# Kernel optimization log

Hardware: AMD Instinct MI355X
Metric: run time of the kernel (lower is better)

## Reference

```python
import jax, jax.numpy as jnp
import numpy as np
from jax.scipy.stats import norm

N = 6144
D1, D2 = 3000, 1000
H = 128          # hardcoded hidden in VAEEncoder
LAT = 64
E = 16           # num_experts
K = 2            # top-k
NOISE_EPS = 0.01
BN_EPS = 1e-5


def setup_inputs() -> dict:
    key = jax.random.key(0)
    ks = jax.random.split(key, 24)
    xav = lambda k, i, o: jax.random.uniform(k, (i, o), jnp.float32,
                                             -np.sqrt(6.0 / (i + o)), np.sqrt(6.0 / (i + o)))
    u = jax.random.uniform(ks[0], (N, N), jnp.float32)
    adj = u / u.sum(axis=1, keepdims=True)  # row-normalized dense graph
    inp = {
        'x1': jax.random.normal(ks[1], (N, D1), jnp.float32),
        'x2': jax.random.normal(ks[2], (N, D2), jnp.float32),
        'adj': adj,
        # modality-1 VAE encoder
        'W1': xav(ks[3], D1, H), 'gamma1': jnp.ones((H,)), 'beta1': jnp.zeros((H,)),
        'Wmu1': xav(ks[4], H, LAT), 'bmu1': jnp.zeros((LAT,)),
        'Wlv1': xav(ks[5], H, LAT), 'blv1': jnp.zeros((LAT,)),
        # modality-2 VAE encoder
        'W2': xav(ks[6], D2, H), 'gamma2': jnp.ones((H,)), 'beta2': jnp.zeros((H,)),
        'Wmu2': xav(ks[7], H, LAT), 'bmu2': jnp.zeros((LAT,)),
        'Wlv2': xav(ks[8], H, LAT), 'blv2': jnp.zeros((LAT,)),
        # MoE gating (torch inits these to zero; small randn gives a non-degenerate baseline)
        'w_gate': 0.02 * jax.random.normal(ks[9], (LAT, E), jnp.float32),
        'w_noise': 0.02 * jax.random.normal(ks[10], (LAT, E), jnp.float32),
        # modality decoders
        'Wd1': xav(ks[11], LAT, LAT), 'Wfc1': xav(ks[12], LAT, D1), 'bfc1': jnp.zeros((D1,)),
        'Wd2': xav(ks[13], LAT, LAT), 'Wfc2': xav(ks[14], LAT, D2), 'bfc2': jnp.zeros((D2,)),
    }
    return inp


def _encode(x, adj, W, gamma, beta, Wmu, bmu, Wlv, blv):
    h = adj @ (x @ W)                                   # [N,H] GNN embed
    mu_b = h.mean(0)
    var_b = h.var(0)
    h = (h - mu_b) / jnp.sqrt(var_b + BN_EPS) * gamma + beta  # BatchNorm1d (train mode)
    return h @ Wmu + bmu, h @ Wlv + blv                 # mu, logvar [N,LAT]


def _cv_squared(v):
    return v.var(ddof=1) / (v.mean() ** 2 + 1e-10)


def _moe_gating(z, w_gate, w_noise, key):
    clean = z @ w_gate                                  # [N,E]
    std = jax.nn.softplus(z @ w_noise) + NOISE_EPS
    noisy = clean + jax.random.normal(key, clean.shape, clean.dtype) * std
    top_vals, top_idx = jax.lax.top_k(noisy, K + 1)     # [N,K+1]
    topk_gates = jax.nn.softmax(top_vals[:, :K], axis=1)
    rows = jnp.arange(z.shape[0])[:, None]
    gates = jnp.zeros_like(clean).at[rows, top_idx[:, :K]].set(topk_gates)
    # differentiable load estimate (prob each expert is in top-k)
    thr_in = top_vals[:, K][:, None]
    thr_out = top_vals[:, K - 1][:, None]
    is_in = noisy > thr_in
    prob = jnp.where(is_in, norm.cdf((clean - thr_in) / std), norm.cdf((clean - thr_out) / std))
    load = prob.sum(0)
    importance = gates.sum(0)
    loss = _cv_squared(importance) + _cv_squared(load)
    return gates, loss


def _decode(z, adj, Wd, Wfc, bfc):
    return (adj @ (z @ Wd)) @ Wfc + bfc                 # Decoder: mm, mm, Linear


def reference(x1, x2, adj,
              W1, gamma1, beta1, Wmu1, bmu1, Wlv1, blv1,
              W2, gamma2, beta2, Wmu2, bmu2, Wlv2, blv2,
              w_gate, w_noise,
              Wd1, Wfc1, bfc1, Wd2, Wfc2, bfc2):
    mu1, lv1 = _encode(x1, adj, W1, gamma1, beta1, Wmu1, bmu1, Wlv1, blv1)
    mu2, lv2 = _encode(x2, adj, W2, gamma2, beta2, Wmu2, bmu2, Wlv2, blv2)
    # Product of Experts over the 2 modalities
    mus = jnp.stack([mu1, mu2], 0)
    lvs = jnp.stack([lv1, lv2], 0)
    var = jnp.exp(lvs) + 1e-8
    T = 1.0 / (var + 1e-8)
    pd_mu = (mus * T).sum(0) / T.sum(0)
    pd_logvar = jnp.log(1.0 / T.sum(0) + 1e-8)
    z = pd_mu
    gates, moe_loss = _moe_gating(z, w_gate, w_noise, jax.random.key(42))
    recon1 = _decode(z, adj, Wd1, Wfc1, bfc1)
    recon2 = _decode(z, adj, Wd2, Wfc2, bfc2)
    return recon1, recon2, pd_mu, pd_logvar, gates, moe_loss
```

## Files before the change

### kernel.cpp

```cpp
#include <hip/hip_runtime.h>
#include <math.h>

#define NR    6144
#define DIM1  3000
#define DIM2  1000
#define HID   128
#define LATD  64
#define NEXP  16

typedef __bf16 bf16x8 __attribute__((ext_vector_type(8)));
typedef float  f32x4  __attribute__((ext_vector_type(4)));

__device__ __forceinline__ unsigned short f2bf_rne(float x) {
  unsigned u = __float_as_uint(x);
  u += 0x7FFFu + ((u >> 16) & 1u);
  return (unsigned short)(u >> 16);
}
__device__ __forceinline__ void split2(float v, unsigned short& h, unsigned short& l) {
  h = f2bf_rne(v);
  float hf = __uint_as_float((unsigned)h << 16);
  l = f2bf_rne(v - hf);
}

template<bool SPLIT3, bool ATOMIC>
__global__ __launch_bounds__(256, 2) void gemm_mfma(
    const float* __restrict__ A,
    const unsigned short* __restrict__ BTh,
    const unsigned short* __restrict__ BTl,
    const float* __restrict__ bias,
    float* __restrict__ C,
    int M, int N, int K, int lda, int Kpad, int ldc, int kchunk)
{
  constexpr int LSZ = 128 * 32;
  __shared__ alignas(16) unsigned short Ah[LSZ];
  __shared__ alignas(16) unsigned short Bh[LSZ];
  __shared__ alignas(16) unsigned short Al[SPLIT3 ? LSZ : 8];
  __shared__ alignas(16) unsigned short Bl[SPLIT3 ? LSZ : 8];

  const int tid  = threadIdx.x;
  const int lane = tid & 63;
  const int wave = tid >> 6;
  const int wm = wave >> 1, wn = wave & 1;
  const int lrow = lane & 15, kg = lane >> 4;

  const int bm = blockIdx.x * 128;
  const int bn = blockIdx.y * 128;
  const int k0 = blockIdx.z * kchunk;
  const int kend = min(k0 + kchunk, K);
  const int nsteps = (kend - k0 + 31) >> 5;

  f32x4 acc[4][4];
  #pragma unroll
  for (int f = 0; f < 4; ++f)
    #pragma unroll
    for (int g = 0; g < 4; ++g)
      #pragma unroll
      for (int j = 0; j < 4; ++j) acc[f][g][j] = 0.f;

  const int srow  = tid >> 1;
  const int ks    = (tid & 1) * 16;
  const int slot0 = (tid & 1) * 2;
  const float* aRow = A + (size_t)(bm + srow) * lda;
  const int gn = bn + srow;
  const bool bvalid = gn < N;
  const unsigned short* bRowH = BTh + (size_t)(bvalid ? gn : 0) * Kpad;
  const unsigned short* bRowL = SPLIT3 ? (BTl + (size_t)(bvalid ? gn : 0) * Kpad) : BTh;

  const int aw0 = srow * 32 + (((slot0    ) ^ (srow & 3)) * 8);
  const int aw1 = srow * 32 + (((slot0 + 1) ^ (srow & 3)) * 8);

  for (int s = 0; s < nsteps; ++s) {
    const int gk = k0 + s * 32;
    const int kb = gk + ks;

    float v[16];
    if (kb + 16 <= kend) {
      const float4* ap = (const float4*)(aRow + kb);
      #pragma unroll
      for (int q = 0; q < 4; ++q) {
        float4 f4 = ap[q];
        v[4*q+0] = f4.x; v[4*q+1] = f4.y; v[4*q+2] = f4.z; v[4*q+3] = f4.w;
      }
    } else {
      #pragma unroll
      for (int i = 0; i < 16; ++i) v[i] = (kb + i < kend) ? aRow[kb + i] : 0.f;
    }
    unsigned hw[8], lw[8];
    #pragma unroll
    for (int i = 0; i < 8; ++i) {
      unsigned short h0, l0, h1, l1;
      split2(v[2*i], h0, l0);
      split2(v[2*i+1], h1, l1);
      hw[i] = (unsigned)h0 | ((unsigned)h1 << 16);
      lw[i] = (unsigned)l0 | ((unsigned)l1 << 16);
    }

    uint4 bh0 = make_uint4(0,0,0,0), bh1 = bh0, bl0 = bh0, bl1 = bh0;
    if (bvalid) {
      const uint4* bp = (const uint4*)(bRowH + gk + ks);
      bh0 = bp[0]; bh1 = bp[1];
      if (SPLIT3) {
        const uint4* bq = (const uint4*)(bRowL + gk + ks);
        bl0 = bq[0]; bl1 = bq[1];
      }
    }

    __syncthreads();
    *(uint4*)&Ah[aw0] = make_uint4(hw[0], hw[1], hw[2], hw[3]);
    *(uint4*)&Ah[aw1] = make_uint4(hw[4], hw[5], hw[6], hw[7]);
    *(uint4*)&Bh[aw0] = bh0;
    *(uint4*)&Bh[aw1] = bh1;
    if (SPLIT3) {
      *(uint4*)&Al[aw0] = make_uint4(lw[0], lw[1], lw[2], lw[3]);
      *(uint4*)&Al[aw1] = make_uint4(lw[4], lw[5], lw[6], lw[7]);
      *(uint4*)&Bl[aw0] = bl0;
      *(uint4*)&Bl[aw1] = bl1;
    }
    __syncthreads();

    bf16x8 afh[4], bfh[4], afl[4], bfl[4];
    #pragma unroll
    for (int f = 0; f < 4; ++f) {
      const int r   = wm * 64 + f * 16 + lrow;
      const int off = r * 32 + ((kg ^ (r & 3)) * 8);
      afh[f] = *(const bf16x8*)&Ah[off];
      const int n    = wn * 64 + f * 16 + lrow;
      const int offb = n * 32 + ((kg ^ (n & 3)) * 8);
      bfh[f] = *(const bf16x8*)&Bh[offb];
      if (SPLIT3) {
        afl[f] = *(const bf16x8*)&Al[off];
        bfl[f] = *(const bf16x8*)&Bl[offb];
      }
    }
    #pragma unroll
    for (int f = 0; f < 4; ++f)
      #pragma unroll
      for (int g = 0; g < 4; ++g) {
        acc[f][g] = __builtin_amdgcn_mfma_f32_16x16x32_bf16(afh[f], bfh[g], acc[f][g], 0, 0, 0);
        if constexpr (SPLIT3) {
          acc[f][g] = __builtin_amdgcn_mfma_f32_16x16x32_bf16(afl[f], bfh[g], acc[f][g], 0, 0, 0);
          acc[f][g] = __builtin_amdgcn_mfma_f32_16x16x32_bf16(afh[f], bfl[g], acc[f][g], 0, 0, 0);
        }
      }
  }

  #pragma unroll
  for (int f = 0; f < 4; ++f) {
    #pragma unroll
    for (int g = 0; g < 4; ++g) {
      const int row0 = bm + wm * 64 + f * 16 + (lane >> 4) * 4;
      const int col  = bn + wn * 64 + g * 16 + (lane & 15);
      if (col < N) {
        #pragma unroll
        for (int j = 0; j < 4; ++j) {
          const size_t idx = (size_t)(row0 + j) * ldc + col;
          if (ATOMIC) atomicAdd(&C[idx], acc[f][g][j]);
          else        C[idx] = acc[f][g][j] + (bias ? bias[col] : 0.f);
        }
      }
    }
  }
}

__global__ __launch_bounds__(256) void transpose_split(
    const float* __restrict__ in, unsigned short* __restrict__ out_hi,
    unsigned short* __restrict__ out_lo, int K, int N, int Kpad)
{
  __shared__ float tile[32][33];
  const int k0 = blockIdx.x * 32, n0 = blockIdx.y * 32;
  const int tx = threadIdx.x & 31, ty = threadIdx.x >> 5;
  #pragma unroll
  for (int r = 0; r < 4; ++r) {
    const int k = k0 + ty + r * 8;
    tile[ty + r * 8][tx] = (k < K && n0 + tx < N) ? in[(size_t)k * N + n0 + tx] : 0.f;
  }
  __syncthreads();
  #pragma unroll
  for (int r = 0; r < 4; ++r) {
    const int nn = ty + r * 8;
    const int n = n0 + nn, k = k0 + tx;
    if (n < N && k < Kpad) {
      unsigned short h, l;
      split2(tile[tx][nn], h, l);
      out_hi[(size_t)n * Kpad + k] = h;
      if (out_lo) out_lo[(size_t)n * Kpad + k] = l;
    }
  }
}

#define BM 64
#define BN 64
#define BK 16

__global__ __launch_bounds__(256) void gemm_f32(
    const float* __restrict__ A, const float* __restrict__ B,
    const float* __restrict__ bias, float* __restrict__ C,
    int M, int N, int K, int lda, int ldb, int ldc)
{
  __shared__ float At[BK][BM + 4];
  __shared__ float Bt[BK][BN + 4];
  const int tid = threadIdx.x;
  const int tx = tid & 15;
  const int ty = tid >> 4;
  const int bm = blockIdx.x * BM;
  const int bn = blockIdx.y * BN;

  float acc[4][4] = {};

  const int ar = tid >> 2;
  const int ak = (tid & 3) * 4;
  const int bk = tid >> 4;
  const int bc = (tid & 15) * 4;

  for (int k0 = 0; k0 < K; k0 += BK) {
    {
      float4 v = make_float4(0.f, 0.f, 0.f, 0.f);
      const int gr = bm + ar;
      const int gk = k0 + ak;
      if (gr < M && gk < K) {
        const float* p = &A[(size_t)gr * lda];
        if (gk + 3 < K) v = *reinterpret_cast<const float4*>(&p[gk]);
        else {
          v.x = p[gk];
          if (gk + 1 < K) v.y = p[gk + 1];
          if (gk + 2 < K) v.z = p[gk + 2];
        }
      }
      At[ak + 0][ar] = v.x; At[ak + 1][ar] = v.y;
      At[ak + 2][ar] = v.z; At[ak + 3][ar] = v.w;
    }
    {
      float4 v = make_float4(0.f, 0.f, 0.f, 0.f);
      const int gk = k0 + bk;
      const int gc = bn + bc;
      if (gk < K) {
        const float* p = &B[(size_t)gk * ldb];
        if (gc + 3 < N) v = *reinterpret_cast<const float4*>(&p[gc]);
        else {
          if (gc     < N) v.x = p[gc];
          if (gc + 1 < N) v.y = p[gc + 1];
          if (gc + 2 < N) v.z = p[gc + 2];
        }
      }
      *reinterpret_cast<float4*>(&Bt[bk][bc]) = v;
    }
    __syncthreads();
    #pragma unroll
    for (int kk = 0; kk < BK; ++kk) {
      float4 a4 = *reinterpret_cast<const float4*>(&At[kk][ty * 4]);
      float4 b4 = *reinterpret_cast<const float4*>(&Bt[kk][tx * 4]);
      float av[4] = {a4.x, a4.y, a4.z, a4.w};
      float bv[4] = {b4.x, b4.y, b4.z, b4.w};
      #pragma unroll
      for (int i = 0; i < 4; ++i)
        #pragma unroll
        for (int j = 0; j < 4; ++j)
          acc[i][j] = fmaf(av[i], bv[j], acc[i][j]);
    }
    __syncthreads();
  }

  #pragma unroll
  for (int i = 0; i < 4; ++i) {
    const int row = bm + ty * 4 + i;
    if (row >= M) continue;
    #pragma unroll
    for (int j = 0; j < 4; ++j) {
      const int col = bn + tx * 4 + j;
      if (col < N) {
        float v = acc[i][j];
        if (bias) v += bias[col];
        C[(size_t)row * ldc + col] = v;
      }
    }
  }
}

__global__ __launch_bounds__(256) void bnstats_kernel(
    const float* __restrict__ H2, float* __restrict__ ssum, float* __restrict__ ssq)
{
  const int c = threadIdx.x;
  const int r0 = blockIdx.x * 12;
  float s = 0.f, q = 0.f;
  #pragma unroll
  for (int i = 0; i < 12; ++i) {
    float v = H2[(size_t)(r0 + i) * 256 + c];
    s += v;
    q = fmaf(v, v, q);
  }
  atomicAdd(&ssum[c], s);
  atomicAdd(&ssq[c], q);
}

__global__ __launch_bounds__(256) void mulv_kernel(
    const float* __restrict__ H2, const float* __restrict__ ssum, const float* __restrict__ ssq,
    const float* __restrict__ g1, const float* __restrict__ b1,
    const float* __restrict__ Wmu1, const float* __restrict__ bmu1,
    const float* __restrict__ Wlv1, const float* __restrict__ blv1,
    const float* __restrict__ g2, const float* __restrict__ b2,
    const float* __restrict__ Wmu2, const float* __restrict__ bmu2,
    const float* __restrict__ Wlv2, const float* __restrict__ blv2,
    float* __restrict__ pd_mu_out, float* __restrict__ pd_lv_out, float* __restrict__ z_out)
{
  __shared__ float hn[4][256];
  const int tid = threadIdx.x;
  const int r0 = blockIdx.x * 4;

  for (int idx = tid; idx < 1024; idx += 256) {
    const int rr = idx >> 8;
    const int c  = idx & 255;
    const float mean = ssum[c] * (1.0f / 6144.0f);
    const float var  = ssq[c] * (1.0f / 6144.0f) - mean * mean;
    const float rstd = 1.0f / sqrtf(var + 1e-5f);
    const float gamma = (c < HID) ? g1[c] : g2[c - HID];
    const float beta  = (c < HID) ? b1[c] : b2[c - HID];
    const float v = H2[(size_t)(r0 + rr) * 256 + c];
    hn[rr][c] = (v - mean) * rstd * gamma + beta;
  }
  __syncthreads();

  const int rr = tid >> 6;
  const int j  = tid & 63;
  float mu1 = bmu1[j], lv1 = blv1[j], mu2 = bmu2[j], lv2 = blv2[j];
  #pragma unroll 4
  for (int k = 0; k < HID; ++k) {
    const float h1 = hn[rr][k];
    const float h2 = hn[rr][HID + k];
    mu1 = fmaf(h1, Wmu1[k * LATD + j], mu1);
    lv1 = fmaf(h1, Wlv1[k * LATD + j], lv1);
    mu2 = fmaf(h2, Wmu2[k * LATD + j], mu2);
    lv2 = fmaf(h2, Wlv2[k * LATD + j], lv2);
  }
  const float var1 = expf(lv1) + 1e-8f;
  const float var2 = expf(lv2) + 1e-8f;
  const float T1 = 1.0f / (var1 + 1e-8f);
  const float T2 = 1.0f / (var2 + 1e-8f);
  const float denom = T1 + T2;
  const float pmu = (mu1 * T1 + mu2 * T2) / denom;
  const float plv = logf(1.0f / denom + 1e-8f);
  const size_t o = (size_t)(r0 + rr) * LATD + j;
  pd_mu_out[o] = pmu;
  pd_lv_out[o] = plv;
  z_out[o]     = pmu;
}

__device__ __forceinline__ unsigned rotl32(unsigned x, int r) {
  return (x << r) | (x >> (32 - r));
}

__device__ float threefry_normal(unsigned i) {
  const unsigned ks0 = 0u;
  const unsigned ks1 = 42u;
  const unsigned ks2 = 0x1BD11BDAu ^ 0u ^ 42u;
  unsigned x0 = 0u + ks0;
  unsigned x1 = i + ks1;

  #define TF_ROUND(r) { x0 += x1; x1 = rotl32(x1, r); x1 ^= x0; }
  TF_ROUND(13) TF_ROUND(15) TF_ROUND(26) TF_ROUND(6)
  x0 += ks1; x1 += ks2 + 1u;
  TF_ROUND(17) TF_ROUND(29) TF_ROUND(16) TF_ROUND(24)
  x0 += ks2; x1 += ks0 + 2u;
  TF_ROUND(13) TF_ROUND(15) TF_ROUND(26) TF_ROUND(6)
  x0 += ks0; x1 += ks1 + 3u;
  TF_ROUND(17) TF_ROUND(29) TF_ROUND(16) TF_ROUND(24)
  x0 += ks1; x1 += ks2 + 4u;
  TF_ROUND(13) TF_ROUND(15) TF_ROUND(26) TF_ROUND(6)
  x0 += ks2; x1 += ks0 + 5u;
  #undef TF_ROUND

  const unsigned bits = x0 ^ x1;

  const unsigned fb = (bits >> 9) | 0x3F800000u;
  const float u01 = __uint_as_float(fb) - 1.0f;
  const float minval = -0.99999994f;
  float u = fmaf(u01, 2.0f, minval);
  u = fmaxf(minval, u);

  float w = -log1pf(-u * u);
  float p;
  if (w < 5.0f) {
    w = w - 2.5f;
    p = 2.81022636e-08f;
    p = fmaf(p, w, 3.43273939e-07f);
    p = fmaf(p, w, -3.5233877e-06f);
    p = fmaf(p, w, -4.39150654e-06f);
    p = fmaf(p, w, 0.00021858087f);
    p = fmaf(p, w, -0.00125372503f);
    p = fmaf(p, w, -0.00417768164f);
    p = fmaf(p, w, 0.246640727f);
    p = fmaf(p, w, 1.50140941f);
  } else {
    w = sqrtf(w) - 3.0f;
    p = -0.000200214257f;
    p = fmaf(p, w, 0.000100950558f);
    p = fmaf(p, w, 0.00134934322f);
    p = fmaf(p, w, -0.00367342844f);
    p = fmaf(p, w, 0.00573950773f);
    p = fmaf(p, w, -0.0076224613f);
    p = fmaf(p, w, 0.00943887047f);
    p = fmaf(p, w, 1.00167406f);
    p = fmaf(p, w, 2.83297682f);
  }
  return 1.4142135f * (p * u);
}

__global__ __launch_bounds__(64) void gating_kernel(
    const float* __restrict__ z, const float* __restrict__ w_gate,
    const float* __restrict__ w_noise, float* __restrict__ gates_out,
    float* __restrict__ importance, float* __restrict__ loadv)
{
  __shared__ float zt[64][65];
  __shared__ float wg[64][16];
  __shared__ float wn[64][16];
  __shared__ float imp_s[16];
  __shared__ float load_s[16];

  const int tid = threadIdx.x;
  const int r0 = blockIdx.x * 64;

  for (int idx = tid; idx < 1024; idx += 64) {
    wg[idx >> 4][idx & 15] = w_gate[idx];
    wn[idx >> 4][idx & 15] = w_noise[idx];
  }
  for (int idx = tid; idx < 4096; idx += 64) {
    const int rr = idx >> 6, c = idx & 63;
    zt[rr][c] = z[(size_t)(r0 + rr) * 64 + c];
  }
  if (tid < 16) { imp_s[tid] = 0.f; load_s[tid] = 0.f; }
  __syncthreads();

  const int r = r0 + tid;
  float clean[16], noisy[16], stdv[16];
  #pragma unroll
  for (int e = 0; e < NEXP; ++e) {
    float c = 0.f, n = 0.f;
    #pragma unroll 8
    for (int k = 0; k < 64; ++k) {
      const float zv = zt[tid][k];
      c = fmaf(zv, wg[k][e], c);
      n = fmaf(zv, wn[k][e], n);
    }
    clean[e] = c;
    const float sp = fmaxf(n, 0.f) + log1pf(expf(-fabsf(n)));
    stdv[e] = sp + 0.01f;
    const float eps = threefry_normal((unsigned)r * 16u + (unsigned)e);
    noisy[e] = fmaf(eps, stdv[e], c);
  }

  float v0 = -1e30f, v1 = -1e30f, v2 = -1e30f;
  int i0 = 0, i1 = 0;
  #pragma unroll
  for (int e = 0; e < NEXP; ++e) {
    const float v = noisy[e];
    if (v > v0)      { v2 = v1; v1 = v0; i1 = i0; v0 = v; i0 = e; }
    else if (v > v1) { v2 = v1; v1 = v; i1 = e; }
    else if (v > v2) { v2 = v; }
  }

  const float e1 = expf(v1 - v0);
  const float inv = 1.0f / (1.0f + e1);
  const float g0 = inv;
  const float g1v = e1 * inv;

  float lacc[16];
  #pragma unroll
  for (int e = 0; e < NEXP; ++e) {
    const float gv = (e == i0) ? g0 : ((e == i1) ? g1v : 0.f);
    gates_out[(size_t)r * NEXP + e] = gv;
    const float thr = (noisy[e] > v2) ? v2 : v1;
    const float x = (clean[e] - thr) / stdv[e];
    lacc[e] = 0.5f * erfcf(-0.70710678f * x);
  }
  atomicAdd(&imp_s[i0], g0);
  atomicAdd(&imp_s[i1], g1v);
  #pragma unroll
  for (int e = 0; e < NEXP; ++e) atomicAdd(&load_s[e], lacc[e]);
  __syncthreads();
  if (tid < 16) {
    atomicAdd(&importance[tid], imp_s[tid]);
    atomicAdd(&loadv[tid], load_s[tid]);
  }
}

__global__ void loss_kernel(const float* __restrict__ imp, const float* __restrict__ ld,
                            float* __restrict__ out)
{
  if (threadIdx.x == 0 && blockIdx.x == 0) {
    float mi = 0.f, ml = 0.f;
    for (int e = 0; e < NEXP; ++e) { mi += imp[e]; ml += ld[e]; }
    mi *= (1.0f / 16.0f);
    ml *= (1.0f / 16.0f);
    float vi = 0.f, vl = 0.f;
    for (int e = 0; e < NEXP; ++e) {
      const float di = imp[e] - mi;
      const float dl = ld[e] - ml;
      vi = fmaf(di, di, vi);
      vl = fmaf(dl, dl, vl);
    }
    vi *= (1.0f / 15.0f);
    vl *= (1.0f / 15.0f);
    out[0] = vi / (mi * mi + 1e-10f) + vl / (ml * ml + 1e-10f);
  }
}

extern "C" void kernel_launch(void* const* d_in, const int* in_sizes, int n_in,
                              void* d_out, int out_size, void* d_ws, size_t ws_size,
                              hipStream_t stream)
{
  const float* x1     = (const float*)d_in[0];
  const float* x2     = (const float*)d_in[1];
  const float* adj    = (const float*)d_in[2];
  const float* W1     = (const float*)d_in[3];
  const float* gamma1 = (const float*)d_in[4];
  const float* beta1  = (const float*)d_in[5];
  const float* Wmu1   = (const float*)d_in[6];
  const float* bmu1   = (const float*)d_in[7];
  const float* Wlv1   = (const float*)d_in[8];
  const float* blv1   = (const float*)d_in[9];
  const float* W2     = (const float*)d_in[10];
  const float* gamma2 = (const float*)d_in[11];
  const float* beta2  = (const float*)d_in[12];
  const float* Wmu2   = (const float*)d_in[13];
  const float* bmu2   = (const float*)d_in[14];
  const float* Wlv2   = (const float*)d_in[15];
  const float* blv2   = (const float*)d_in[16];
  const float* w_gate = (const float*)d_in[17];
  const float* w_noise= (const float*)d_in[18];
  const float* Wd1    = (const float*)d_in[19];
  const float* Wfc1   = (const float*)d_in[20];
  const float* bfc1   = (const float*)d_in[21];
  const float* Wd2    = (const float*)d_in[22];
  const float* Wfc2   = (const float*)d_in[23];
  const float* bfc2   = (const float*)d_in[24];

  float* out = (float*)d_out;
  float* recon1 = out;
  float* recon2 = out + (size_t)NR * DIM1;
  float* pd_mu  = recon2 + (size_t)NR * DIM2;
  float* pd_lv  = pd_mu + (size_t)NR * LATD;
  float* gates  = pd_lv + (size_t)NR * LATD;
  float* loss   = gates + (size_t)NR * NEXP;

  char* wsb = (char*)d_ws;
  const size_t o_XW   = 0;
  const size_t o_H2   = o_XW   + 6291456;
  const size_t o_z    = o_H2   + 6291456;
  const size_t o_ZD   = o_z    + 1572864;
  const size_t o_AZ   = o_ZD   + 3145728;
  const size_t o_XWTh = o_AZ   + 3145728;
  const size_t o_XWTl = o_XWTh + 3145728;
  const size_t o_W1Th = o_XWTl + 3145728;
  const size_t o_W1Tl = o_W1Th + 770048;
  const size_t o_W2Th = o_W1Tl + 770048;
  const size_t o_W2Tl = o_W2Th + 262144;
  const size_t o_ZDTh = o_W2Tl + 262144;
  const size_t o_F1Th = o_ZDTh + 1572864;
  const size_t o_F2Th = o_F1Th + 384000;
  const size_t o_stat = o_F2Th + 128000;
  const size_t need   = o_stat + 2176;

  const dim3 blk(256);

  if (ws_size >= need) {
    float* XW   = (float*)(wsb + o_XW);
    float* H2   = (float*)(wsb + o_H2);
    float* zbuf = (float*)(wsb + o_z);
    float* ZD   = (float*)(wsb + o_ZD);
    float* AZ   = (float*)(wsb + o_AZ);
    unsigned short* XWTh = (unsigned short*)(wsb + o_XWTh);
    unsigned short* XWTl = (unsigned short*)(wsb + o_XWTl);
    unsigned short* W1Th = (unsigned short*)(wsb + o_W1Th);
    unsigned short* W1Tl = (unsigned short*)(wsb + o_W1Tl);
    unsigned short* W2Th = (unsigned short*)(wsb + o_W2Th);
    unsigned short* W2Tl = (unsigned short*)(wsb + o_W2Tl);
    unsigned short* ZDTh = (unsigned short*)(wsb + o_ZDTh);
    unsigned short* F1Th = (unsigned short*)(wsb + o_F1Th);
    unsigned short* F2Th = (unsigned short*)(wsb + o_F2Th);
    float* ssum = (float*)(wsb + o_stat);
    float* ssq  = ssum + 256;
    float* imp  = ssq + 256;
    float* ldv  = imp + 16;

    hipMemsetAsync(XW, 0, 6291456 * 2, stream);
    hipMemsetAsync(AZ, 0, 3145728, stream);
    hipMemsetAsync(ssum, 0, 2176, stream);

    transpose_split<<<dim3(94, 4), blk, 0, stream>>>(W1, W1Th, W1Tl, DIM1, HID, 3008);
    transpose_split<<<dim3(32, 4), blk, 0, stream>>>(W2, W2Th, W2Tl, DIM2, HID, 1024);
    transpose_split<<<dim3(2, 94), blk, 0, stream>>>(Wfc1, F1Th, nullptr, LATD, DIM1, 64);
    transpose_split<<<dim3(2, 32), blk, 0, stream>>>(Wfc2, F2Th, nullptr, LATD, DIM2, 64);

    gemm_mfma<true, true><<<dim3(48, 1, 4), blk, 0, stream>>>(
        x1, W1Th, W1Tl, nullptr, XW, NR, HID, DIM1, DIM1, 3008, 256, 768);
    gemm_mfma<true, true><<<dim3(48, 1, 4), blk, 0, stream>>>(
        x2, W2Th, W2Tl, nullptr, XW + HID, NR, HID, DIM2, DIM2, 1024, 256, 256);

    transpose_split<<<dim3(192, 8), blk, 0, stream>>>(XW, XWTh, XWTl, NR, 256, NR);

    gemm_mfma<true, true><<<dim3(48, 2, 4), blk, 0, stream>>>(
        adj, XWTh, XWTl, nullptr, H2, NR, 256, NR, NR, NR, 256, 1536);

    bnstats_kernel<<<512, blk, 0, stream>>>(H2, ssum, ssq);
    mulv_kernel<<<NR / 4, blk, 0, stream>>>(H2, ssum, ssq,
        gamma1, beta1, Wmu1, bmu1, Wlv1, blv1,
        gamma2, beta2, Wmu2, bmu2, Wlv2, blv2,
        pd_mu, pd_lv, zbuf);

    gating_kernel<<<NR / 64, 64, 0, stream>>>(zbuf, w_gate, w_noise, gates, imp, ldv);
    loss_kernel<<<1, 64, 0, stream>>>(imp, ldv, loss);

    gemm_f32<<<dim3(96, 1), blk, 0, stream>>>(zbuf, Wd1, nullptr, ZD,        NR, LATD, LATD, LATD, LATD, 128);
    gemm_f32<<<dim3(96, 1), blk, 0, stream>>>(zbuf, Wd2, nullptr, ZD + LATD, NR, LATD, LATD, LATD, LATD, 128);
    transpose_split<<<dim3(192, 4), blk, 0, stream>>>(ZD, ZDTh, nullptr, NR, 128, NR);
    gemm_mfma<false, true><<<dim3(48, 1, 4), blk, 0, stream>>>(
        adj, ZDTh, nullptr, nullptr, AZ, NR, 128, NR, NR, NR, 128, 1536);
    gemm_mfma<false, false><<<dim3(48, 24, 1), blk, 0, stream>>>(
        AZ, F1Th, nullptr, bfc1, recon1, NR, DIM1, LATD, 128, 64, DIM1, 64);
    gemm_mfma<false, false><<<dim3(48, 8, 1), blk, 0, stream>>>(
        AZ + LATD, F2Th, nullptr, bfc2, recon2, NR, DIM2, LATD, 128, 64, DIM2, 64);
    return;
  }

  float* ws   = (float*)d_ws;
  float* XW   = ws;
  float* H2   = ws + 1572864;
  float* zbuf = ws + 3145728;
  float* ZD   = ws + 3538944;
  float* AZ   = ws + 4325376;
  float* ssum = ws + 5111808;
  float* ssq  = ws + 5112064;
  float* imp  = ws + 5112320;
  float* ldv  = ws + 5112336;

  hipMemsetAsync(ssum, 0, 544 * sizeof(float), stream);

  gemm_f32<<<dim3(NR / BM, 2), blk, 0, stream>>>(x1, W1, nullptr, XW,        NR, HID, DIM1, DIM1, HID, 256);
  gemm_f32<<<dim3(NR / BM, 2), blk, 0, stream>>>(x2, W2, nullptr, XW + HID,  NR, HID, DIM2, DIM2, HID, 256);
  gemm_f32<<<dim3(NR / BM, 4), blk, 0, stream>>>(adj, XW, nullptr, H2, NR, 256, NR, NR, 256, 256);
  bnstats_kernel<<<512, blk, 0, stream>>>(H2, ssum, ssq);
  mulv_kernel<<<NR / 4, blk, 0, stream>>>(H2, ssum, ssq,
                                          gamma1, beta1, Wmu1, bmu1, Wlv1, blv1,
                                          gamma2, beta2, Wmu2, bmu2, Wlv2, blv2,
                                          pd_mu, pd_lv, zbuf);
  gating_kernel<<<NR / 64, 64, 0, stream>>>(zbuf, w_gate, w_noise, gates, imp, ldv);
  loss_kernel<<<1, 64, 0, stream>>>(imp, ldv, loss);
  gemm_f32<<<dim3(NR / BM, 1), blk, 0, stream>>>(zbuf, Wd1, nullptr, ZD,        NR, LATD, LATD, LATD, LATD, 128);
  gemm_f32<<<dim3(NR / BM, 1), blk, 0, stream>>>(zbuf, Wd2, nullptr, ZD + LATD, NR, LATD, LATD, LATD, LATD, 128);
  gemm_f32<<<dim3(NR / BM, 2), blk, 0, stream>>>(adj, ZD, nullptr, AZ, NR, 128, NR, NR, 128, 128);
  gemm_f32<<<dim3(NR / BM, (DIM1 + BN - 1) / BN), blk, 0, stream>>>(AZ,        Wfc1, bfc1, recon1, NR, DIM1, LATD, 128, DIM1, DIM1);
  gemm_f32<<<dim3(NR / BM, (DIM2 + BN - 1) / BN), blk, 0, stream>>>(AZ + LATD, Wfc2, bfc2, recon2, NR, DIM2, LATD, 128, DIM2, DIM2);
}
```

Before: 482.9 us.

## Merge encoder GEMMs, double split-K, and repack LDS tiles into shared buffers

The two encoder input GEMMs are fused into one launch that picks the modality by blockIdx.y, with split-K raised to 8 chunks. The large adj GEMMs also move from 4 to 8 K-chunks, which gives more blocks to fill the CUs. LDS is repacked so the hi/lo halves share one 64-wide swizzled row, and the non-split path stores A and B in one buffer, cutting shared memory use. The cost is more atomic adds into the output and more partial-sum traffic.

```diff
diff --git a/kernel.cpp b/kernel.cpp
--- a/kernel.cpp
+++ b/kernel.cpp
@@ -23,30 +23,21 @@
 }
 
 template<bool SPLIT3, bool ATOMIC>
-__global__ __launch_bounds__(256, 2) void gemm_mfma(
+__device__ __forceinline__ void gemm_body(
+    unsigned short* __restrict__ bufA, unsigned short* __restrict__ bufB,
     const float* __restrict__ A,
     const unsigned short* __restrict__ BTh,
     const unsigned short* __restrict__ BTl,
     const float* __restrict__ bias,
     float* __restrict__ C,
-    int M, int N, int K, int lda, int Kpad, int ldc, int kchunk)
-{
-  constexpr int LSZ = 128 * 32;
-  __shared__ alignas(16) unsigned short Ah[LSZ];
-  __shared__ alignas(16) unsigned short Bh[LSZ];
-  __shared__ alignas(16) unsigned short Al[SPLIT3 ? LSZ : 8];
-  __shared__ alignas(16) unsigned short Bl[SPLIT3 ? LSZ : 8];
-
+    int M, int N, int K, int lda, int Kpad, int ldc,
+    int bm, int bn, int k0, int kend)
+{
   const int tid  = threadIdx.x;
   const int lane = tid & 63;
   const int wave = tid >> 6;
   const int wm = wave >> 1, wn = wave & 1;
   const int lrow = lane & 15, kg = lane >> 4;
-
-  const int bm = blockIdx.x * 128;
-  const int bn = blockIdx.y * 128;
-  const int k0 = blockIdx.z * kchunk;
-  const int kend = min(k0 + kchunk, K);
   const int nsteps = (kend - k0 + 31) >> 5;
 
   f32x4 acc[4][4];
@@ -57,17 +48,20 @@
       #pragma unroll
       for (int j = 0; j < 4; ++j) acc[f][g][j] = 0.f;
 
-  const int srow  = tid >> 1;
-  const int ks    = (tid & 1) * 16;
-  const int slot0 = (tid & 1) * 2;
+  const int srow = tid >> 1;
+  const int ks   = (tid & 1) * 16;
+  const int s0   = (tid & 1) * 2;
   const float* aRow = A + (size_t)(bm + srow) * lda;
   const int gn = bn + srow;
   const bool bvalid = gn < N;
   const unsigned short* bRowH = BTh + (size_t)(bvalid ? gn : 0) * Kpad;
   const unsigned short* bRowL = SPLIT3 ? (BTl + (size_t)(bvalid ? gn : 0) * Kpad) : BTh;
 
-  const int aw0 = srow * 32 + (((slot0    ) ^ (srow & 3)) * 8);
-  const int aw1 = srow * 32 + (((slot0 + 1) ^ (srow & 3)) * 8);
+  const int rx = srow & 7;
+  const int wa0 = srow * 64 + (((s0 + 0) ^ rx) * 8);
+  const int wa1 = srow * 64 + (((s0 + 1) ^ rx) * 8);
+  const int wa2 = srow * 64 + (((s0 + 4) ^ rx) * 8);
+  const int wa3 = srow * 64 + (((s0 + 5) ^ rx) * 8);
 
   for (int s = 0; s < nsteps; ++s) {
     const int gk = k0 + s * 32;
@@ -88,11 +82,16 @@
     unsigned hw[8], lw[8];
     #pragma unroll
     for (int i = 0; i < 8; ++i) {
-      unsigned short h0, l0, h1, l1;
-      split2(v[2*i], h0, l0);
-      split2(v[2*i+1], h1, l1);
-      hw[i] = (unsigned)h0 | ((unsigned)h1 << 16);
-      lw[i] = (unsigned)l0 | ((unsigned)l1 << 16);
+      if (SPLIT3) {
+        unsigned short h0, l0, h1, l1;
+        split2(v[2*i], h0, l0);
+        split2(v[2*i+1], h1, l1);
+        hw[i] = (unsigned)h0 | ((unsigned)h1 << 16);
+        lw[i] = (unsigned)l0 | ((unsigned)l1 << 16);
+      } else {
+        hw[i] = (unsigned)f2bf_rne(v[2*i]) | ((unsigned)f2bf_rne(v[2*i+1]) << 16);
+        lw[i] = 0;
+      }
     }
 
     uint4 bh0 = make_uint4(0,0,0,0), bh1 = bh0, bl0 = bh0, bl1 = bh0;
@@ -106,30 +105,33 @@
     }
 
     __syncthreads();
-    *(uint4*)&Ah[aw0] = make_uint4(hw[0], hw[1], hw[2], hw[3]);
-    *(uint4*)&Ah[aw1] = make_uint4(hw[4], hw[5], hw[6], hw[7]);
-    *(uint4*)&Bh[aw0] = bh0;
-    *(uint4*)&Bh[aw1] = bh1;
+    *(uint4*)&bufA[wa0] = make_uint4(hw[0], hw[1], hw[2], hw[3]);
+    *(uint4*)&bufA[wa1] = make_uint4(hw[4], hw[5], hw[6], hw[7]);
     if (SPLIT3) {
-      *(uint4*)&Al[aw0] = make_uint4(lw[0], lw[1], lw[2], lw[3]);
-      *(uint4*)&Al[aw1] = make_uint4(lw[4], lw[5], lw[6], lw[7]);
-      *(uint4*)&Bl[aw0] = bl0;
-      *(uint4*)&Bl[aw1] = bl1;
+      *(uint4*)&bufA[wa2] = make_uint4(lw[0], lw[1], lw[2], lw[3]);
+      *(uint4*)&bufA[wa3] = make_uint4(lw[4], lw[5], lw[6], lw[7]);
+      *(uint4*)&bufB[wa0] = bh0;
+      *(uint4*)&bufB[wa1] = bh1;
+      *(uint4*)&bufB[wa2] = bl0;
+      *(uint4*)&bufB[wa3] = bl1;
+    } else {
+      *(uint4*)&bufA[wa2] = bh0;
+      *(uint4*)&bufA[wa3] = bh1;
     }
     __syncthreads();
 
     bf16x8 afh[4], bfh[4], afl[4], bfl[4];
     #pragma unroll
     for (int f = 0; f < 4; ++f) {
-      const int r   = wm * 64 + f * 16 + lrow;
-      const int off = r * 32 + ((kg ^ (r & 3)) * 8);
-      afh[f] = *(const bf16x8*)&Ah[off];
-      const int n    = wn * 64 + f * 16 + lrow;
-      const int offb = n * 32 + ((kg ^ (n & 3)) * 8);
-      bfh[f] = *(const bf16x8*)&Bh[offb];
+      const int r = wm * 64 + f * 16 + lrow;
+      afh[f] = *(const bf16x8*)&bufA[r * 64 + ((kg ^ (r & 7)) * 8)];
+      if (SPLIT3) afl[f] = *(const bf16x8*)&bufA[r * 64 + (((4 + kg) ^ (r & 7)) * 8)];
+      const int n = wn * 64 + f * 16 + lrow;
       if (SPLIT3) {
-        afl[f] = *(const bf16x8*)&Al[off];
-        bfl[f] = *(const bf16x8*)&Bl[offb];
+        bfh[f] = *(const bf16x8*)&bufB[n * 64 + ((kg ^ (n & 7)) * 8)];
+        bfl[f] = *(const bf16x8*)&bufB[n * 64 + (((4 + kg) ^ (n & 7)) * 8)];
+      } else {
+        bfh[f] = *(const bf16x8*)&bufA[n * 64 + (((4 + kg) ^ (n & 7)) * 8)];
       }
     }
     #pragma unroll
@@ -159,6 +161,46 @@
         }
       }
     }
+  }
+}
+
+template<bool SPLIT3, bool ATOMIC>
+__global__ __launch_bounds__(256, 2) void gemm_mfma(
+    const float* __restrict__ A,
+    const unsigned short* __restrict__ BTh,
+    const unsigned short* __restrict__ BTl,
+    const float* __restrict__ bias,
+    float* __restrict__ C,
+    int M, int N, int K, int lda, int Kpad, int ldc, int kchunk)
+{
+  __shared__ alignas(16) unsigned short bufA[128 * 64];
+  __shared__ alignas(16) unsigned short bufB[SPLIT3 ? 128 * 64 : 8];
+  const int k0 = blockIdx.z * kchunk;
+  gemm_body<SPLIT3, ATOMIC>(bufA, bufB, A, BTh, BTl, bias, C,
+                            M, N, K, lda, Kpad, ldc,
+                            blockIdx.x * 128, blockIdx.y * 128,
+                            k0, min(k0 + kchunk, K));
+}
+
+__global__ __launch_bounds__(256, 2) void gemm_enc(
+    const float* __restrict__ x1,
+    const unsigned short* __restrict__ W1h, const unsigned short* __restrict__ W1l,
+    const float* __restrict__ x2,
+    const unsigned short* __restrict__ W2h, const unsigned short* __restrict__ W2l,
+    float* __restrict__ XW)
+{
+  __shared__ alignas(16) unsigned short bufA[128 * 64];
+  __shared__ alignas(16) unsigned short bufB[128 * 64];
+  if (blockIdx.y == 0) {
+    const int k0 = blockIdx.z * 376;
+    gemm_body<true, true>(bufA, bufB, x1, W1h, W1l, nullptr, XW,
+                          NR, HID, DIM1, DIM1, 3008, 256,
+                          blockIdx.x * 128, 0, k0, min(k0 + 376, DIM1));
+  } else {
+    const int k0 = blockIdx.z * 128;
+    gemm_body<true, true>(bufA, bufB, x2, W2h, W2l, nullptr, XW + HID,
+                          NR, HID, DIM2, DIM2, 1024, 256,
+                          blockIdx.x * 128, 0, k0, min(k0 + 128, DIM2));
   }
 }
 
@@ -590,15 +632,12 @@
     transpose_split<<<dim3(2, 94), blk, 0, stream>>>(Wfc1, F1Th, nullptr, LATD, DIM1, 64);
     transpose_split<<<dim3(2, 32), blk, 0, stream>>>(Wfc2, F2Th, nullptr, LATD, DIM2, 64);
 
-    gemm_mfma<true, true><<<dim3(48, 1, 4), blk, 0, stream>>>(
-        x1, W1Th, W1Tl, nullptr, XW, NR, HID, DIM1, DIM1, 3008, 256, 768);
-    gemm_mfma<true, true><<<dim3(48, 1, 4), blk, 0, stream>>>(
-        x2, W2Th, W2Tl, nullptr, XW + HID, NR, HID, DIM2, DIM2, 1024, 256, 256);
+    gemm_enc<<<dim3(48, 2, 8), blk, 0, stream>>>(x1, W1Th, W1Tl, x2, W2Th, W2Tl, XW);
 
     transpose_split<<<dim3(192, 8), blk, 0, stream>>>(XW, XWTh, XWTl, NR, 256, NR);
 
-    gemm_mfma<true, true><<<dim3(48, 2, 4), blk, 0, stream>>>(
-        adj, XWTh, XWTl, nullptr, H2, NR, 256, NR, NR, NR, 256, 1536);
+    gemm_mfma<true, true><<<dim3(48, 2, 8), blk, 0, stream>>>(
+        adj, XWTh, XWTl, nullptr, H2, NR, 256, NR, NR, NR, 256, 768);
 
     bnstats_kernel<<<512, blk, 0, stream>>>(H2, ssum, ssq);
     mulv_kernel<<<NR / 4, blk, 0, stream>>>(H2, ssum, ssq,
@@ -612,8 +651,8 @@
     gemm_f32<<<dim3(96, 1), blk, 0, stream>>>(zbuf, Wd1, nullptr, ZD,        NR, LATD, LATD, LATD, LATD, 128);
     gemm_f32<<<dim3(96, 1), blk, 0, stream>>>(zbuf, Wd2, nullptr, ZD + LATD, NR, LATD, LATD, LATD, LATD, 128);
     transpose_split<<<dim3(192, 4), blk, 0, stream>>>(ZD, ZDTh, nullptr, NR, 128, NR);
-    gemm_mfma<false, true><<<dim3(48, 1, 4), blk, 0, stream>>>(
-        adj, ZDTh, nullptr, nullptr, AZ, NR, 128, NR, NR, NR, 128, 1536);
+    gemm_mfma<false, true><<<dim3(48, 1, 8), blk, 0, stream>>>(
+        adj, ZDTh, nullptr, nullptr, AZ, NR, 128, NR, NR, NR, 128, 768);
     gemm_mfma<false, false><<<dim3(48, 24, 1), blk, 0, stream>>>(
         AZ, F1Th, nullptr, bfc1, recon1, NR, DIM1, LATD, 128, 64, DIM1, 64);
     gemm_mfma<false, false><<<dim3(48, 8, 1), blk, 0, stream>>>(
```

Result: faster. 418.6 us (-13.3%).
